# Kernel optimization log

Hardware: AMD Instinct MI355X
Metric: run time of the kernel (lower is better)

The kernel has to match this reference:

```python
import jax, jax.numpy as jnp
import numpy as np


def setup_inputs() -> dict:
    key = jax.random.key(0)
    ks = jax.random.split(key, 7)
    B, S, D, H, Dh = 4, 2048, 1024, 16, 64
    return {
        "query_input": jax.random.normal(ks[0], (B, S, D), jnp.float32),
        "key_input": jax.random.normal(ks[1], (B, S, D), jnp.float32),
        "value_input": jax.random.normal(ks[2], (B, S, D), jnp.float32),
        "Wq": jax.random.normal(ks[3], (D, H, Dh), jnp.float32) * 0.03,
        "Wk": jax.random.normal(ks[4], (D, H, Dh), jnp.float32) * 0.03,
        "Wv": jax.random.normal(ks[5], (D, H, Dh), jnp.float32) * 0.03,
        "Wo": jax.random.normal(ks[6], (H, Dh, D), jnp.float32) * 0.03,
    }


def reference(query_input, key_input, value_input, Wq, Wk, Wv, Wo):
    # Projections: [B,S,D] x [D,H,Dh] -> [B,S,H,Dh]
    q = jnp.einsum("bsd,dhk->bshk", query_input, Wq)
    k = jnp.einsum("bsd,dhk->bshk", key_input, Wk)
    v = jnp.einsum("bsd,dhk->bshk", value_input, Wv)
    depth = Wq.shape[-1]
    q = q * (depth ** -0.5)
    # logits: [B,H,F,T]  (F = query len, T = key len)
    logits = jnp.einsum("bthk,bfhk->bhft", k, q)
    weights = jax.nn.softmax(logits, axis=-1)
    # attention output: [B,F,H,Dh]
    ctx = jnp.einsum("bhft,bthk->bfhk", weights, v)
    # output projection: [B,F,H,Dh] x [H,Dh,D] -> [B,F,D]
    return jnp.einsum("bfhk,hkd->bfd", ctx, Wo)
```

## Files before the change

kernel.cpp:

```cpp
#include <hip/hip_runtime.h>
#include <stdint.h>

typedef __bf16 bf16;
typedef __bf16 bf16x4 __attribute__((ext_vector_type(4)));
typedef __bf16 bf16x8 __attribute__((ext_vector_type(8)));
typedef float f32x4 __attribute__((ext_vector_type(4)));

#define AS1 __attribute__((address_space(1)))
#define AS3 __attribute__((address_space(3)))

__device__ __forceinline__ void async16(void* lds, const void* g) {
    __builtin_amdgcn_global_load_lds((AS1 void*)g, (AS3 void*)lds, 16, 0, 0);
}

__global__ __launch_bounds__(256) void prep(
    const float* __restrict__ x0, const float* __restrict__ x1,
    const float* __restrict__ x2,
    bf16* __restrict__ y0, bf16* __restrict__ y1, bf16* __restrict__ y2,
    const float* __restrict__ s0, const float* __restrict__ s1,
    const float* __restrict__ s2, const float* __restrict__ s3,
    bf16* __restrict__ d0, bf16* __restrict__ d1,
    bf16* __restrict__ d2, bf16* __restrict__ d3) {
    const int z = blockIdx.z;
    const int t = threadIdx.x;
    if (z < 3) {
        const float* x = z == 0 ? x0 : z == 1 ? x1 : x2;
        bf16* y = z == 0 ? y0 : z == 1 ? y1 : y2;
        int i = (blockIdx.x * 256 + t) * 8;
        f32x4 a = *(const f32x4*)(x + i);
        f32x4 b = *(const f32x4*)(x + i + 4);
        bf16x8 o;
#pragma unroll
        for (int j = 0; j < 4; ++j) { o[j] = (bf16)a[j]; o[4 + j] = (bf16)b[j]; }
        *(bf16x8*)(y + i) = o;
        return;
    }
    const int bx = blockIdx.x;
    if (bx >= 1024) return;
    const int wsel = bx >> 8, tile = bx & 255;
    const float* W = wsel == 0 ? s0 : wsel == 1 ? s1 : wsel == 2 ? s2 : s3;
    bf16* Wt = wsel == 0 ? d0 : wsel == 1 ? d1 : wsel == 2 ? d2 : d3;
    const int k0 = (tile >> 4) * 64, n0 = (tile & 15) * 64;
    __shared__ float Ts[64 * 65];
    const int c = t & 63, r0 = t >> 6;
#pragma unroll
    for (int i = 0; i < 16; ++i) {
        int r = r0 + i * 4;
        Ts[r * 65 + c] = W[(size_t)(k0 + r) * 1024 + n0 + c];
    }
    __syncthreads();
#pragma unroll
    for (int i = 0; i < 16; ++i) {
        int r = r0 + i * 4;
        Wt[(size_t)(n0 + r) * 1024 + k0 + c] = (bf16)Ts[c * 65 + r];
    }
}

template <typename OutT>
__device__ __forceinline__ void gemm_body(const bf16* __restrict__ A,
                                          const bf16* __restrict__ Bt,
                                          OutT* __restrict__ C,
                                          int N, int K, float scale,
                                          int m0, int n0,
                                          bf16* As, bf16* Bs) {
    const int t = threadIdx.x;
    const int lane = t & 63;
    const int w = t >> 6;
    const int l15 = lane & 15;
    const int quad = lane >> 4;
    const int wm = w >> 1, wn = w & 1;

    f32x4 acc[4][4];
#pragma unroll
    for (int i = 0; i < 4; ++i)
#pragma unroll
        for (int j = 0; j < 4; ++j) acc[i][j] = (f32x4){0.f, 0.f, 0.f, 0.f};

    const bf16* gA[4];
    const bf16* gB[4];
#pragma unroll
    for (int j = 0; j < 4; ++j) {
        int c = j * 256 + t;
        int row = c >> 3, g = (c & 7) ^ (row & 7);
        gA[j] = A + (size_t)(m0 + row) * K + g * 8;
        gB[j] = Bt + (size_t)(n0 + row) * K + g * 8;
    }

    for (int k0 = 0; k0 < K; k0 += 64) {
        __syncthreads();
#pragma unroll
        for (int j = 0; j < 4; ++j) {
            async16(As + (j * 256 + w * 64) * 8, gA[j] + k0);
            async16(Bs + (j * 256 + w * 64) * 8, gB[j] + k0);
        }
        __syncthreads();
#pragma unroll
        for (int kk = 0; kk < 2; ++kk) {
            bf16x8 af[4], bfv[4];
#pragma unroll
            for (int mi = 0; mi < 4; ++mi) {
                int r = wm * 64 + mi * 16 + l15;
                af[mi] = *(const bf16x8*)&As[r * 64 + (((kk * 4 + quad) ^ (r & 7)) * 8)];
            }
#pragma unroll
            for (int ni = 0; ni < 4; ++ni) {
                int r = wn * 64 + ni * 16 + l15;
                bfv[ni] = *(const bf16x8*)&Bs[r * 64 + (((kk * 4 + quad) ^ (r & 7)) * 8)];
            }
#pragma unroll
            for (int mi = 0; mi < 4; ++mi)
#pragma unroll
                for (int ni = 0; ni < 4; ++ni)
                    acc[mi][ni] = __builtin_amdgcn_mfma_f32_16x16x32_bf16(
                        af[mi], bfv[ni], acc[mi][ni], 0, 0, 0);
        }
    }

#pragma unroll
    for (int mi = 0; mi < 4; ++mi)
#pragma unroll
        for (int ni = 0; ni < 4; ++ni)
#pragma unroll
            for (int r = 0; r < 4; ++r) {
                int row = m0 + wm * 64 + mi * 16 + quad * 4 + r;
                int col = n0 + wn * 64 + ni * 16 + l15;
                C[(size_t)row * N + col] = (OutT)(acc[mi][ni][r] * scale);
            }
}

__global__ __launch_bounds__(256) void gemm_qkv(
    const bf16* __restrict__ Xq, const bf16* __restrict__ Xk, const bf16* __restrict__ Xv,
    const bf16* __restrict__ Wqt, const bf16* __restrict__ Wkt, const bf16* __restrict__ Wvt,
    bf16* __restrict__ Qb, bf16* __restrict__ Kb, bf16* __restrict__ VtG) {
    __shared__ __align__(16) bf16 As[128 * 64];
    __shared__ __align__(16) bf16 Bs[128 * 64];
    const int z = blockIdx.z;
    const int blk = blockIdx.x;
    const int big  = (blk & 7) * 8 + (blk >> 6);
    const int sml  = (blk >> 3) & 7;
    const bf16* A; const bf16* Bt; bf16* C; int N; float scale; int m0, n0;
    if (z == 0) { A = Xq; Bt = Wqt; C = Qb; N = 1024; scale = 0.18033688011112042f;
                  m0 = big * 128; n0 = sml * 128; }
    else if (z == 1) { A = Xk; Bt = Wkt; C = Kb; N = 1024; scale = 1.0f;
                  m0 = big * 128; n0 = sml * 128; }
    else { A = Wvt; Bt = Xv; C = VtG; N = 8192; scale = 1.0f;
                  m0 = sml * 128; n0 = big * 128; }
    gemm_body<bf16>(A, Bt, C, N, 1024, scale, m0, n0, As, Bs);
}

__global__ __launch_bounds__(256) void gemm_out(const bf16* __restrict__ A,
                                                const bf16* __restrict__ Bt,
                                                float* __restrict__ C) {
    __shared__ __align__(16) bf16 As[128 * 64];
    __shared__ __align__(16) bf16 Bs[128 * 64];
    const int blk = blockIdx.x;
    const int big = (blk & 7) * 8 + (blk >> 6);
    const int sml = (blk >> 3) & 7;
    gemm_body<float>(A, Bt, C, 1024, 1024, 1.0f, big * 128, sml * 128, As, Bs);
}

__global__ __launch_bounds__(512) void attn_fa(const bf16* __restrict__ Q,
                                               const bf16* __restrict__ K,
                                               const bf16* __restrict__ Vt,
                                               bf16* __restrict__ O) {
    __shared__ __align__(16) bf16 Ks[2][64 * 64];
    __shared__ __align__(16) bf16 Vs[2][64 * 64];
    __shared__ __align__(16) bf16 Pt[8][32 * 64];

    const int t = threadIdx.x;
    const int lane = t & 63;
    const int w = t >> 6;
    const int l15 = lane & 15;
    const int quad = lane >> 4;
    const int q7 = l15 & 7;

    const int bid = blockIdx.x;
    const int bh = (bid & 7) * 8 + ((bid >> 3) & 7);
    const int q0 = (bid >> 6) * 256;
    const int b = bh >> 4, h = bh & 15;
    const size_t baseQ = (size_t)b * 2048 * 1024 + (size_t)h * 64;

    const int r0s = t >> 3, g0s = (t & 7) ^ (r0s & 7);
    const bf16* gK0 = K + baseQ + (size_t)r0s * 1024 + g0s * 8;
    const bf16* gV0 = Vt + (size_t)(h * 64 + r0s) * 8192 + (size_t)b * 2048 + g0s * 8;

    bf16x8 qf[2][2];
#pragma unroll
    for (int mi = 0; mi < 2; ++mi)
#pragma unroll
        for (int kk = 0; kk < 2; ++kk)
            qf[mi][kk] = *(const bf16x8*)(Q + baseQ +
                (size_t)(q0 + w * 32 + mi * 16 + l15) * 1024 + kk * 32 + quad * 8);

    f32x4 accO[4][2];
    float l_part[2] = {0.f, 0.f};
#pragma unroll
    for (int nd = 0; nd < 4; ++nd)
#pragma unroll
        for (int mi = 0; mi < 2; ++mi) accO[nd][mi] = (f32x4){0.f, 0.f, 0.f, 0.f};

    auto swz = [&](int r, int g) { return (r * 8 + (g ^ (r & 7))) * 8; };
    auto stage = [&](int t0, int bi) {
        async16((bf16*)Ks[bi] + w * 512, gK0 + (size_t)t0 * 1024);
        async16((bf16*)Vs[bi] + w * 512, gV0 + t0);
    };

    stage(0, 0);

    for (int it = 0; it < 32; ++it) {
        __syncthreads();
        if (it + 1 < 32) stage((it + 1) * 64, (it + 1) & 1);
        const bf16* Kb = Ks[it & 1];
        const bf16* Vb = Vs[it & 1];

        f32x4 accS[4][2];
#pragma unroll
        for (int nt = 0; nt < 4; ++nt)
#pragma unroll
            for (int mi = 0; mi < 2; ++mi) accS[nt][mi] = (f32x4){0.f, 0.f, 0.f, 0.f};
#pragma unroll
        for (int kk = 0; kk < 2; ++kk) {
            bf16x8 kf[4];
#pragma unroll
            for (int nt = 0; nt < 4; ++nt)
                kf[nt] = *(const bf16x8*)&Kb[swz(nt * 16 + l15, kk * 4 + quad)];
            __builtin_amdgcn_s_setprio(1);
#pragma unroll
            for (int nt = 0; nt < 4; ++nt)
#pragma unroll
                for (int mi = 0; mi < 2; ++mi)
                    accS[nt][mi] = __builtin_amdgcn_mfma_f32_16x16x32_bf16(
                        kf[nt], qf[mi][kk], accS[nt][mi], 0, 0, 0);
            __builtin_amdgcn_s_setprio(0);
        }

        bf16* Pp = &Pt[w][0];
#pragma unroll
        for (int mi = 0; mi < 2; ++mi) {
            const int qbase = (mi * 16 + l15) * 64;
            float rs = 0.f;
#pragma unroll
            for (int nt = 0; nt < 4; ++nt) {
                bf16x4 pk;
#pragma unroll
                for (int r = 0; r < 4; ++r) {
                    float p = __builtin_amdgcn_exp2f(accS[nt][mi][r]);
                    rs += p;
                    pk[r] = (bf16)p;
                }
                *(bf16x4*)&Pp[qbase + (((nt * 2 + (quad >> 1)) ^ q7) * 8) +
                              (quad & 1) * 4] = pk;
            }
            l_part[mi] += rs;
        }

#pragma unroll
        for (int kk = 0; kk < 2; ++kk) {
            bf16x8 vf[4], pf[2];
#pragma unroll
            for (int nd = 0; nd < 4; ++nd)
                vf[nd] = *(const bf16x8*)&Vb[swz(nd * 16 + l15, kk * 4 + quad)];
#pragma unroll
            for (int mi = 0; mi < 2; ++mi)
                pf[mi] = *(const bf16x8*)&Pp[(mi * 16 + l15) * 64 +
                                             (((kk * 4 + quad) ^ q7) * 8)];
            __builtin_amdgcn_s_setprio(1);
#pragma unroll
            for (int nd = 0; nd < 4; ++nd)
#pragma unroll
                for (int mi = 0; mi < 2; ++mi)
                    accO[nd][mi] = __builtin_amdgcn_mfma_f32_16x16x32_bf16(
                        vf[nd], pf[mi], accO[nd][mi], 0, 0, 0);
            __builtin_amdgcn_s_setprio(0);
        }
    }

    float inv[2];
#pragma unroll
    for (int mi = 0; mi < 2; ++mi) {
        float l = l_part[mi];
        l += __shfl_xor(l, 16);
        l += __shfl_xor(l, 32);
        inv[mi] = 1.0f / l;
    }

#pragma unroll
    for (int mi = 0; mi < 2; ++mi) {
        size_t rowoff = baseQ + (size_t)(q0 + w * 32 + mi * 16 + l15) * 1024;
#pragma unroll
        for (int nd = 0; nd < 4; ++nd) {
            bf16x4 o;
#pragma unroll
            for (int r = 0; r < 4; ++r) o[r] = (bf16)(accO[nd][mi][r] * inv[mi]);
            *(bf16x4*)&O[rowoff + nd * 16 + quad * 4] = o;
        }
    }
}

extern "C" void kernel_launch(void* const* d_in, const int* in_sizes, int n_in,
                              void* d_out, int out_size, void* d_ws, size_t ws_size,
                              hipStream_t stream) {
    const float* qin = (const float*)d_in[0];
    const float* kin = (const float*)d_in[1];
    const float* vin = (const float*)d_in[2];
    const float* Wq = (const float*)d_in[3];
    const float* Wk = (const float*)d_in[4];
    const float* Wv = (const float*)d_in[5];
    const float* Wo = (const float*)d_in[6];
    float* out = (float*)d_out;

    char* ws = (char*)d_ws;
    bf16* Xq  = (bf16*)(ws);
    bf16* Xk  = (bf16*)(ws + ((size_t)16 << 20));
    bf16* Xv  = (bf16*)(ws + ((size_t)32 << 20));
    bf16* Qb  = (bf16*)(ws + ((size_t)48 << 20));
    bf16* Kb  = (bf16*)(ws + ((size_t)64 << 20));
    bf16* VtG = (bf16*)(ws + ((size_t)80 << 20));
    bf16* Cb  = (bf16*)(ws);
    bf16* Wqt = (bf16*)(ws + ((size_t)96 << 20));
    bf16* Wkt = Wqt + 1024 * 1024;
    bf16* Wvt = Wkt + 1024 * 1024;
    bf16* Wot = Wvt + 1024 * 1024;

    prep<<<dim3(4096, 1, 4), 256, 0, stream>>>(qin, kin, vin, Xq, Xk, Xv,
                                               Wq, Wk, Wv, Wo, Wqt, Wkt, Wvt, Wot);
    gemm_qkv<<<dim3(512, 1, 3), 256, 0, stream>>>(Xq, Xk, Xv, Wqt, Wkt, Wvt,
                                                  Qb, Kb, VtG);
    attn_fa<<<dim3(512), 512, 0, stream>>>(Qb, Kb, VtG, Cb);
    gemm_out<<<dim3(512), 256, 0, stream>>>(Cb, Wot, out);
}
```

Baseline: 312.6 us.

## Rewrite projection GEMMs with 256-row tiles, double-buffered LDS and interleaved prefetch

Replaces the 128x128 single-buffered GEMM body with a 256x256 (QKV) or 256x128 (output) tile computed by 512 threads. K tiles are double-buffered in LDS, and the async global-to-LDS loads for the next tile are issued between MFMA groups with explicit vmcnt waits and raised wave priority around the MFMAs. The aim is to hide global load latency and to raise arithmetic intensity per LDS byte. In exchange there are fewer blocks (384 and 256), more accumulator registers and 128KB of LDS for the QKV kernel, which may limit occupancy and cause tail imbalance.

```diff
diff --git a/kernel.cpp b/kernel.cpp
--- a/kernel.cpp
+++ b/kernel.cpp
@@ -56,107 +56,225 @@
     }
 }
 
-template <typename OutT>
-__device__ __forceinline__ void gemm_body(const bf16* __restrict__ A,
-                                          const bf16* __restrict__ Bt,
-                                          OutT* __restrict__ C,
-                                          int N, int K, float scale,
-                                          int m0, int n0,
-                                          bf16* As, bf16* Bs) {
+template <int NREP, typename OutT>
+__device__ __forceinline__ void gemm256_body(
+    const bf16* __restrict__ A, const bf16* __restrict__ Bt,
+    OutT* __restrict__ C, int N, float scale, int m0, int n0,
+    bf16* As0, bf16* As1, bf16* Bs0, bf16* Bs1) {
     const int t = threadIdx.x;
     const int lane = t & 63;
     const int w = t >> 6;
     const int l15 = lane & 15;
     const int quad = lane >> 4;
-    const int wm = w >> 1, wn = w & 1;
-
-    f32x4 acc[4][4];
-#pragma unroll
-    for (int i = 0; i < 4; ++i)
-#pragma unroll
-        for (int j = 0; j < 4; ++j) acc[i][j] = (f32x4){0.f, 0.f, 0.f, 0.f};
-
-    const bf16* gA[4];
-    const bf16* gB[4];
+    const int wm = w >> 2, wn = w & 3;
+    constexpr int K = 1024;
+
+    f32x4 acc[8][NREP];
+#pragma unroll
+    for (int i = 0; i < 8; ++i)
+#pragma unroll
+        for (int j = 0; j < NREP; ++j) acc[i][j] = (f32x4){0.f, 0.f, 0.f, 0.f};
+
+    const bf16* pA[4];
+    const bf16* pB[NREP];
 #pragma unroll
     for (int j = 0; j < 4; ++j) {
-        int c = j * 256 + t;
-        int row = c >> 3, g = (c & 7) ^ (row & 7);
-        gA[j] = A + (size_t)(m0 + row) * K + g * 8;
-        gB[j] = Bt + (size_t)(n0 + row) * K + g * 8;
-    }
-
-    for (int k0 = 0; k0 < K; k0 += 64) {
-        __syncthreads();
-#pragma unroll
-        for (int j = 0; j < 4; ++j) {
-            async16(As + (j * 256 + w * 64) * 8, gA[j] + k0);
-            async16(Bs + (j * 256 + w * 64) * 8, gB[j] + k0);
-        }
-        __syncthreads();
-#pragma unroll
-        for (int kk = 0; kk < 2; ++kk) {
-            bf16x8 af[4], bfv[4];
-#pragma unroll
-            for (int mi = 0; mi < 4; ++mi) {
-                int r = wm * 64 + mi * 16 + l15;
-                af[mi] = *(const bf16x8*)&As[r * 64 + (((kk * 4 + quad) ^ (r & 7)) * 8)];
-            }
-#pragma unroll
-            for (int ni = 0; ni < 4; ++ni) {
-                int r = wn * 64 + ni * 16 + l15;
-                bfv[ni] = *(const bf16x8*)&Bs[r * 64 + (((kk * 4 + quad) ^ (r & 7)) * 8)];
-            }
+        int c = j * 512 + t, row = c >> 3, g = (c & 7) ^ (row & 7);
+        pA[j] = A + (size_t)(m0 + row) * K + g * 8;
+    }
+#pragma unroll
+    for (int j = 0; j < NREP; ++j) {
+        int c = j * 512 + t, row = c >> 3, g = (c & 7) ^ (row & 7);
+        pB[j] = Bt + (size_t)(n0 + row) * K + g * 8;
+    }
+    bf16* AsB[2] = {As0, As1};
+    bf16* BsB[2] = {Bs0, Bs1};
+
+#pragma unroll
+    for (int j = 0; j < 4; ++j) {
+        async16(As0 + (j * 512 + w * 64) * 8, pA[j]); pA[j] += 64;
+    }
+#pragma unroll
+    for (int j = 0; j < NREP; ++j) {
+        async16(Bs0 + (j * 512 + w * 64) * 8, pB[j]); pB[j] += 64;
+    }
+
+    for (int tt = 0; tt < 16; ++tt) {
+        const int cb = tt & 1, ob = cb ^ 1;
+        const bf16* Acur = AsB[cb];
+        const bf16* Bcur = BsB[cb];
+        bf16* Anxt = AsB[ob];
+        bf16* Bnxt = BsB[ob];
+        const bool pf = tt < 15;
+
+        if (pf) {
+            async16(Anxt + (0 * 512 + w * 64) * 8, pA[0]); pA[0] += 64;
+            async16(Anxt + (1 * 512 + w * 64) * 8, pA[1]); pA[1] += 64;
+            async16(Bnxt + (0 * 512 + w * 64) * 8, pB[0]); pB[0] += 64;
+            async16(Bnxt + (1 * 512 + w * 64) * 8, pB[1]); pB[1] += 64;
+            asm volatile("s_waitcnt vmcnt(4)" ::: "memory");
+        } else {
+            asm volatile("s_waitcnt vmcnt(0)" ::: "memory");
+        }
+        __builtin_amdgcn_s_barrier();
+
+        bf16x8 aF[8];
+        bf16x8 bF[NREP * 2];
+
+#pragma unroll
+        for (int mi = 0; mi < 4; ++mi)
+#pragma unroll
+            for (int kk = 0; kk < 2; ++kk) {
+                int r = wm * 128 + mi * 16 + l15;
+                aF[mi * 2 + kk] =
+                    *(const bf16x8*)&Acur[r * 64 + (((kk * 4 + quad) ^ (r & 7)) * 8)];
+            }
+#pragma unroll
+        for (int ni = 0; ni < 2; ++ni)
+#pragma unroll
+            for (int kk = 0; kk < 2; ++kk) {
+                int r = wn * (NREP * 16) + ni * 16 + l15;
+                bF[ni * 2 + kk] =
+                    *(const bf16x8*)&Bcur[r * 64 + (((kk * 4 + quad) ^ (r & 7)) * 8)];
+            }
+        __builtin_amdgcn_s_setprio(1);
+#pragma unroll
+        for (int mi = 0; mi < 4; ++mi)
+#pragma unroll
+            for (int ni = 0; ni < 2; ++ni)
+#pragma unroll
+                for (int kk = 0; kk < 2; ++kk)
+                    acc[mi][ni] = __builtin_amdgcn_mfma_f32_16x16x32_bf16(
+                        aF[mi * 2 + kk], bF[ni * 2 + kk], acc[mi][ni], 0, 0, 0);
+        __builtin_amdgcn_s_setprio(0);
+
+        if constexpr (NREP == 4) {
+#pragma unroll
+            for (int ni = 2; ni < 4; ++ni)
+#pragma unroll
+                for (int kk = 0; kk < 2; ++kk) {
+                    int r = wn * 64 + ni * 16 + l15;
+                    bF[ni * 2 + kk] =
+                        *(const bf16x8*)&Bcur[r * 64 + (((kk * 4 + quad) ^ (r & 7)) * 8)];
+                }
+            if (pf) {
+                async16(Anxt + (2 * 512 + w * 64) * 8, pA[2]); pA[2] += 64;
+                async16(Anxt + (3 * 512 + w * 64) * 8, pA[3]); pA[3] += 64;
+            }
+            __builtin_amdgcn_s_setprio(1);
 #pragma unroll
             for (int mi = 0; mi < 4; ++mi)
 #pragma unroll
-                for (int ni = 0; ni < 4; ++ni)
-                    acc[mi][ni] = __builtin_amdgcn_mfma_f32_16x16x32_bf16(
-                        af[mi], bfv[ni], acc[mi][ni], 0, 0, 0);
-        }
-    }
-
-#pragma unroll
-    for (int mi = 0; mi < 4; ++mi)
-#pragma unroll
-        for (int ni = 0; ni < 4; ++ni)
+                for (int ni = 2; ni < 4; ++ni)
+#pragma unroll
+                    for (int kk = 0; kk < 2; ++kk)
+                        acc[mi][ni] = __builtin_amdgcn_mfma_f32_16x16x32_bf16(
+                            aF[mi * 2 + kk], bF[ni * 2 + kk], acc[mi][ni], 0, 0, 0);
+            __builtin_amdgcn_s_setprio(0);
+
+#pragma unroll
+            for (int mi = 0; mi < 4; ++mi)
+#pragma unroll
+                for (int kk = 0; kk < 2; ++kk) {
+                    int r = wm * 128 + (mi + 4) * 16 + l15;
+                    aF[mi * 2 + kk] =
+                        *(const bf16x8*)&Acur[r * 64 + (((kk * 4 + quad) ^ (r & 7)) * 8)];
+                }
+            if (pf) {
+                async16(Bnxt + (2 * 512 + w * 64) * 8, pB[2]); pB[2] += 64;
+                async16(Bnxt + (3 * 512 + w * 64) * 8, pB[3]); pB[3] += 64;
+            }
+            __builtin_amdgcn_s_setprio(1);
+#pragma unroll
+            for (int mi = 4; mi < 8; ++mi)
+#pragma unroll
+                for (int ni = 2; ni < 4; ++ni)
+#pragma unroll
+                    for (int kk = 0; kk < 2; ++kk)
+                        acc[mi][ni] = __builtin_amdgcn_mfma_f32_16x16x32_bf16(
+                            aF[(mi & 3) * 2 + kk], bF[ni * 2 + kk], acc[mi][ni], 0, 0, 0);
+            __builtin_amdgcn_s_setprio(0);
+
+            __builtin_amdgcn_s_setprio(1);
+#pragma unroll
+            for (int mi = 4; mi < 8; ++mi)
+#pragma unroll
+                for (int ni = 0; ni < 2; ++ni)
+#pragma unroll
+                    for (int kk = 0; kk < 2; ++kk)
+                        acc[mi][ni] = __builtin_amdgcn_mfma_f32_16x16x32_bf16(
+                            aF[(mi & 3) * 2 + kk], bF[ni * 2 + kk], acc[mi][ni], 0, 0, 0);
+            __builtin_amdgcn_s_setprio(0);
+        } else {
+#pragma unroll
+            for (int mi = 0; mi < 4; ++mi)
+#pragma unroll
+                for (int kk = 0; kk < 2; ++kk) {
+                    int r = wm * 128 + (mi + 4) * 16 + l15;
+                    aF[mi * 2 + kk] =
+                        *(const bf16x8*)&Acur[r * 64 + (((kk * 4 + quad) ^ (r & 7)) * 8)];
+                }
+            if (pf) {
+                async16(Anxt + (2 * 512 + w * 64) * 8, pA[2]); pA[2] += 64;
+                async16(Anxt + (3 * 512 + w * 64) * 8, pA[3]); pA[3] += 64;
+            }
+            __builtin_amdgcn_s_setprio(1);
+#pragma unroll
+            for (int mi = 4; mi < 8; ++mi)
+#pragma unroll
+                for (int ni = 0; ni < 2; ++ni)
+#pragma unroll
+                    for (int kk = 0; kk < 2; ++kk)
+                        acc[mi][ni] = __builtin_amdgcn_mfma_f32_16x16x32_bf16(
+                            aF[(mi & 3) * 2 + kk], bF[ni * 2 + kk], acc[mi][ni], 0, 0, 0);
+            __builtin_amdgcn_s_setprio(0);
+        }
+
+        asm volatile("s_waitcnt lgkmcnt(0)" ::: "memory");
+        __builtin_amdgcn_s_barrier();
+    }
+
+#pragma unroll
+    for (int mi = 0; mi < 8; ++mi)
+#pragma unroll
+        for (int ni = 0; ni < NREP; ++ni)
 #pragma unroll
             for (int r = 0; r < 4; ++r) {
-                int row = m0 + wm * 64 + mi * 16 + quad * 4 + r;
-                int col = n0 + wn * 64 + ni * 16 + l15;
+                int row = m0 + wm * 128 + mi * 16 + quad * 4 + r;
+                int col = n0 + wn * (NREP * 16) + ni * 16 + l15;
                 C[(size_t)row * N + col] = (OutT)(acc[mi][ni][r] * scale);
             }
 }
 
-__global__ __launch_bounds__(256) void gemm_qkv(
+__global__ __launch_bounds__(512, 2) void gemm_qkv(
     const bf16* __restrict__ Xq, const bf16* __restrict__ Xk, const bf16* __restrict__ Xv,
     const bf16* __restrict__ Wqt, const bf16* __restrict__ Wkt, const bf16* __restrict__ Wvt,
     bf16* __restrict__ Qb, bf16* __restrict__ Kb, bf16* __restrict__ VtG) {
-    __shared__ __align__(16) bf16 As[128 * 64];
-    __shared__ __align__(16) bf16 Bs[128 * 64];
+    __shared__ __align__(16) bf16 As[2][256 * 64];
+    __shared__ __align__(16) bf16 Bs[2][256 * 64];
     const int z = blockIdx.z;
-    const int blk = blockIdx.x;
-    const int big  = (blk & 7) * 8 + (blk >> 6);
-    const int sml  = (blk >> 3) & 7;
+    const int x = blockIdx.x;
+    const int sml = (x & 7) >> 1;
+    const int big = (x >> 3) * 2 + (x & 1);
     const bf16* A; const bf16* Bt; bf16* C; int N; float scale; int m0, n0;
     if (z == 0) { A = Xq; Bt = Wqt; C = Qb; N = 1024; scale = 0.18033688011112042f;
-                  m0 = big * 128; n0 = sml * 128; }
+                  m0 = big * 256; n0 = sml * 256; }
     else if (z == 1) { A = Xk; Bt = Wkt; C = Kb; N = 1024; scale = 1.0f;
-                  m0 = big * 128; n0 = sml * 128; }
+                  m0 = big * 256; n0 = sml * 256; }
     else { A = Wvt; Bt = Xv; C = VtG; N = 8192; scale = 1.0f;
-                  m0 = sml * 128; n0 = big * 128; }
-    gemm_body<bf16>(A, Bt, C, N, 1024, scale, m0, n0, As, Bs);
-}
-
-__global__ __launch_bounds__(256) void gemm_out(const bf16* __restrict__ A,
-                                                const bf16* __restrict__ Bt,
-                                                float* __restrict__ C) {
-    __shared__ __align__(16) bf16 As[128 * 64];
-    __shared__ __align__(16) bf16 Bs[128 * 64];
-    const int blk = blockIdx.x;
-    const int big = (blk & 7) * 8 + (blk >> 6);
-    const int sml = (blk >> 3) & 7;
-    gemm_body<float>(A, Bt, C, 1024, 1024, 1.0f, big * 128, sml * 128, As, Bs);
+                  m0 = sml * 256; n0 = big * 256; }
+    gemm256_body<4, bf16>(A, Bt, C, N, scale, m0, n0, As[0], As[1], Bs[0], Bs[1]);
+}
+
+__global__ __launch_bounds__(512, 2) void gemm_out(const bf16* __restrict__ A,
+                                                   const bf16* __restrict__ Bt,
+                                                   float* __restrict__ C) {
+    __shared__ __align__(16) bf16 As[2][256 * 64];
+    __shared__ __align__(16) bf16 Bs[2][128 * 64];
+    const int x = blockIdx.x;
+    const int bm = x >> 3, bn = x & 7;
+    gemm256_body<2, float>(A, Bt, C, 1024, 1.0f, bm * 256, bn * 128,
+                           As[0], As[1], Bs[0], Bs[1]);
 }
 
 __global__ __launch_bounds__(512) void attn_fa(const bf16* __restrict__ Q,
@@ -324,8 +442,8 @@
 
     prep<<<dim3(4096, 1, 4), 256, 0, stream>>>(qin, kin, vin, Xq, Xk, Xv,
                                                Wq, Wk, Wv, Wo, Wqt, Wkt, Wvt, Wot);
-    gemm_qkv<<<dim3(512, 1, 3), 256, 0, stream>>>(Xq, Xk, Xv, Wqt, Wkt, Wvt,
+    gemm_qkv<<<dim3(128, 1, 3), 512, 0, stream>>>(Xq, Xk, Xv, Wqt, Wkt, Wvt,
                                                   Qb, Kb, VtG);
     attn_fa<<<dim3(512), 512, 0, stream>>>(Qb, Kb, VtG, Cb);
-    gemm_out<<<dim3(512), 256, 0, stream>>>(Cb, Wot, out);
-}
+    gemm_out<<<dim3(256), 512, 0, stream>>>(Cb, Wot, out);
+}
```

Measured after the change: 389.6 us. 1.25x slower.

## Fuse fp32-to-bf16 activation conversion into QKV GEMM with register prefetch

Applied to the files above, without the earlier changes.

The separate prep pass that converted the three fp32 activation tensors to bf16 is removed. The QKV GEMM now reads fp32 activations directly, converts them to bf16 in registers and writes them to LDS, prefetching the next K-tile into registers while the MFMAs run. This removes a full read/write round trip of three 32 MB tensors. In exchange, each GEMM block re-reads the fp32 activations once per N-tile, which is twice the bytes of the bf16 copy. The synchronous LDS stores and the explicit waitcnt may also reduce overlap for the paths that still use async loads.

```diff
diff --git a/kernel.cpp b/kernel.cpp
--- a/kernel.cpp
+++ b/kernel.cpp
@@ -14,29 +14,12 @@
 }
 
 __global__ __launch_bounds__(256) void prep(
-    const float* __restrict__ x0, const float* __restrict__ x1,
-    const float* __restrict__ x2,
-    bf16* __restrict__ y0, bf16* __restrict__ y1, bf16* __restrict__ y2,
     const float* __restrict__ s0, const float* __restrict__ s1,
     const float* __restrict__ s2, const float* __restrict__ s3,
     bf16* __restrict__ d0, bf16* __restrict__ d1,
     bf16* __restrict__ d2, bf16* __restrict__ d3) {
-    const int z = blockIdx.z;
+    const int bx = blockIdx.x;
     const int t = threadIdx.x;
-    if (z < 3) {
-        const float* x = z == 0 ? x0 : z == 1 ? x1 : x2;
-        bf16* y = z == 0 ? y0 : z == 1 ? y1 : y2;
-        int i = (blockIdx.x * 256 + t) * 8;
-        f32x4 a = *(const f32x4*)(x + i);
-        f32x4 b = *(const f32x4*)(x + i + 4);
-        bf16x8 o;
-#pragma unroll
-        for (int j = 0; j < 4; ++j) { o[j] = (bf16)a[j]; o[4 + j] = (bf16)b[j]; }
-        *(bf16x8*)(y + i) = o;
-        return;
-    }
-    const int bx = blockIdx.x;
-    if (bx >= 1024) return;
     const int wsel = bx >> 8, tile = bx & 255;
     const float* W = wsel == 0 ? s0 : wsel == 1 ? s1 : wsel == 2 ? s2 : s3;
     bf16* Wt = wsel == 0 ? d0 : wsel == 1 ? d1 : wsel == 2 ? d2 : d3;
@@ -56,9 +39,8 @@
     }
 }
 
-template <typename OutT>
-__device__ __forceinline__ void gemm_body(const bf16* __restrict__ A,
-                                          const bf16* __restrict__ Bt,
+template <int AF32, int BF32, typename OutT>
+__device__ __forceinline__ void gemm_body(const void* Ap, const void* Bp,
                                           OutT* __restrict__ C,
                                           int N, int K, float scale,
                                           int m0, int n0,
@@ -76,24 +58,100 @@
 #pragma unroll
         for (int j = 0; j < 4; ++j) acc[i][j] = (f32x4){0.f, 0.f, 0.f, 0.f};
 
-    const bf16* gA[4];
-    const bf16* gB[4];
+    int crow[4], cg[4];
 #pragma unroll
     for (int j = 0; j < 4; ++j) {
         int c = j * 256 + t;
-        int row = c >> 3, g = (c & 7) ^ (row & 7);
-        gA[j] = A + (size_t)(m0 + row) * K + g * 8;
-        gB[j] = Bt + (size_t)(n0 + row) * K + g * 8;
+        crow[j] = c >> 3;
+        cg[j] = (c & 7) ^ (crow[j] & 7);
+    }
+    const bf16* a16[4]; const float* a32[4];
+    const bf16* b16[4]; const float* b32[4];
+#pragma unroll
+    for (int j = 0; j < 4; ++j) {
+        if constexpr (AF32)
+            a32[j] = (const float*)Ap + (size_t)(m0 + crow[j]) * K + cg[j] * 8;
+        else
+            a16[j] = (const bf16*)Ap + (size_t)(m0 + crow[j]) * K + cg[j] * 8;
+        if constexpr (BF32)
+            b32[j] = (const float*)Bp + (size_t)(n0 + crow[j]) * K + cg[j] * 8;
+        else
+            b16[j] = (const bf16*)Bp + (size_t)(n0 + crow[j]) * K + cg[j] * 8;
+    }
+
+    f32x4 ar[8], br[8];
+    if constexpr (AF32) {
+#pragma unroll
+        for (int j = 0; j < 4; ++j) {
+            ar[2 * j] = *(const f32x4*)a32[j];
+            ar[2 * j + 1] = *(const f32x4*)(a32[j] + 4);
+        }
+    }
+    if constexpr (BF32) {
+#pragma unroll
+        for (int j = 0; j < 4; ++j) {
+            br[2 * j] = *(const f32x4*)b32[j];
+            br[2 * j + 1] = *(const f32x4*)(b32[j] + 4);
+        }
     }
 
     for (int k0 = 0; k0 < K; k0 += 64) {
-        __syncthreads();
-#pragma unroll
-        for (int j = 0; j < 4; ++j) {
-            async16(As + (j * 256 + w * 64) * 8, gA[j] + k0);
-            async16(Bs + (j * 256 + w * 64) * 8, gB[j] + k0);
-        }
-        __syncthreads();
+        __builtin_amdgcn_s_barrier();
+        __builtin_amdgcn_sched_barrier(0);
+
+        if constexpr (AF32) {
+#pragma unroll
+            for (int j = 0; j < 4; ++j) {
+                bf16x8 cv;
+#pragma unroll
+                for (int r = 0; r < 4; ++r) {
+                    cv[r] = (bf16)ar[2 * j][r];
+                    cv[4 + r] = (bf16)ar[2 * j + 1][r];
+                }
+                *(bf16x8*)&As[(j * 256 + t) * 8] = cv;
+            }
+        } else {
+#pragma unroll
+            for (int j = 0; j < 4; ++j) async16(As + (j * 256 + w * 64) * 8, a16[j] + k0);
+        }
+        if constexpr (BF32) {
+#pragma unroll
+            for (int j = 0; j < 4; ++j) {
+                bf16x8 cv;
+#pragma unroll
+                for (int r = 0; r < 4; ++r) {
+                    cv[r] = (bf16)br[2 * j][r];
+                    cv[4 + r] = (bf16)br[2 * j + 1][r];
+                }
+                *(bf16x8*)&Bs[(j * 256 + t) * 8] = cv;
+            }
+        } else {
+#pragma unroll
+            for (int j = 0; j < 4; ++j) async16(Bs + (j * 256 + w * 64) * 8, b16[j] + k0);
+        }
+
+        asm volatile("s_waitcnt vmcnt(0) lgkmcnt(0)" ::: "memory");
+        __builtin_amdgcn_s_barrier();
+        __builtin_amdgcn_sched_barrier(0);
+
+        const bool pf = (k0 + 64 < K);
+        if (pf) {
+            if constexpr (AF32) {
+#pragma unroll
+                for (int j = 0; j < 4; ++j) {
+                    ar[2 * j] = *(const f32x4*)(a32[j] + k0 + 64);
+                    ar[2 * j + 1] = *(const f32x4*)(a32[j] + k0 + 68);
+                }
+            }
+            if constexpr (BF32) {
+#pragma unroll
+                for (int j = 0; j < 4; ++j) {
+                    br[2 * j] = *(const f32x4*)(b32[j] + k0 + 64);
+                    br[2 * j + 1] = *(const f32x4*)(b32[j] + k0 + 68);
+                }
+            }
+        }
+
 #pragma unroll
         for (int kk = 0; kk < 2; ++kk) {
             bf16x8 af[4], bfv[4];
@@ -129,23 +187,26 @@
 }
 
 __global__ __launch_bounds__(256) void gemm_qkv(
-    const bf16* __restrict__ Xq, const bf16* __restrict__ Xk, const bf16* __restrict__ Xv,
-    const bf16* __restrict__ Wqt, const bf16* __restrict__ Wkt, const bf16* __restrict__ Wvt,
+    const float* __restrict__ Xq, const float* __restrict__ Xk,
+    const float* __restrict__ Xv,
+    const bf16* __restrict__ Wqt, const bf16* __restrict__ Wkt,
+    const bf16* __restrict__ Wvt,
     bf16* __restrict__ Qb, bf16* __restrict__ Kb, bf16* __restrict__ VtG) {
     __shared__ __align__(16) bf16 As[128 * 64];
     __shared__ __align__(16) bf16 Bs[128 * 64];
     const int z = blockIdx.z;
     const int blk = blockIdx.x;
-    const int big  = (blk & 7) * 8 + (blk >> 6);
-    const int sml  = (blk >> 3) & 7;
-    const bf16* A; const bf16* Bt; bf16* C; int N; float scale; int m0, n0;
-    if (z == 0) { A = Xq; Bt = Wqt; C = Qb; N = 1024; scale = 0.18033688011112042f;
-                  m0 = big * 128; n0 = sml * 128; }
-    else if (z == 1) { A = Xk; Bt = Wkt; C = Kb; N = 1024; scale = 1.0f;
-                  m0 = big * 128; n0 = sml * 128; }
-    else { A = Wvt; Bt = Xv; C = VtG; N = 8192; scale = 1.0f;
-                  m0 = sml * 128; n0 = big * 128; }
-    gemm_body<bf16>(A, Bt, C, N, 1024, scale, m0, n0, As, Bs);
+    const int big = (blk & 7) * 8 + (blk >> 6);
+    const int sml = (blk >> 3) & 7;
+    if (z == 0)
+        gemm_body<1, 0, bf16>(Xq, Wqt, Qb, 1024, 1024, 0.18033688011112042f,
+                              big * 128, sml * 128, As, Bs);
+    else if (z == 1)
+        gemm_body<1, 0, bf16>(Xk, Wkt, Kb, 1024, 1024, 1.0f,
+                              big * 128, sml * 128, As, Bs);
+    else
+        gemm_body<0, 1, bf16>(Wvt, Xv, VtG, 8192, 1024, 1.0f,
+                              sml * 128, big * 128, As, Bs);
 }
 
 __global__ __launch_bounds__(256) void gemm_out(const bf16* __restrict__ A,
@@ -156,7 +217,8 @@
     const int blk = blockIdx.x;
     const int big = (blk & 7) * 8 + (blk >> 6);
     const int sml = (blk >> 3) & 7;
-    gemm_body<float>(A, Bt, C, 1024, 1024, 1.0f, big * 128, sml * 128, As, Bs);
+    gemm_body<0, 0, float>(A, Bt, C, 1024, 1024, 1.0f, big * 128, sml * 128,
+                           As, Bs);
 }
 
 __global__ __launch_bounds__(512) void attn_fa(const bf16* __restrict__ Q,
@@ -310,9 +372,6 @@
     float* out = (float*)d_out;
 
     char* ws = (char*)d_ws;
-    bf16* Xq  = (bf16*)(ws);
-    bf16* Xk  = (bf16*)(ws + ((size_t)16 << 20));
-    bf16* Xv  = (bf16*)(ws + ((size_t)32 << 20));
     bf16* Qb  = (bf16*)(ws + ((size_t)48 << 20));
     bf16* Kb  = (bf16*)(ws + ((size_t)64 << 20));
     bf16* VtG = (bf16*)(ws + ((size_t)80 << 20));
@@ -322,9 +381,8 @@
     bf16* Wvt = Wkt + 1024 * 1024;
     bf16* Wot = Wvt + 1024 * 1024;
 
-    prep<<<dim3(4096, 1, 4), 256, 0, stream>>>(qin, kin, vin, Xq, Xk, Xv,
-                                               Wq, Wk, Wv, Wo, Wqt, Wkt, Wvt, Wot);
-    gemm_qkv<<<dim3(512, 1, 3), 256, 0, stream>>>(Xq, Xk, Xv, Wqt, Wkt, Wvt,
+    prep<<<dim3(1024), 256, 0, stream>>>(Wq, Wk, Wv, Wo, Wqt, Wkt, Wvt, Wot);
+    gemm_qkv<<<dim3(512, 1, 3), 256, 0, stream>>>(qin, kin, vin, Wqt, Wkt, Wvt,
                                                   Qb, Kb, VtG);
     attn_fa<<<dim3(512), 512, 0, stream>>>(Qb, Kb, VtG, Cb);
     gemm_out<<<dim3(512), 256, 0, stream>>>(Cb, Wot, out);
```

After: 351.6 us. +12.5%, slower.
